# Optimization experiments

Hardware: AMD Instinct MI355X
Metric: run time of the kernel (lower is better)

The kernel has to match this reference:

```python
import jax, jax.numpy as jnp
import numpy as np

EPS = 1e-5

def setup_inputs() -> dict:
    key = jax.random.key(0)
    B, T, C, H = 1, 4096, 1024, 16
    ks = jax.random.split(key, 8)
    s = lambda k, sh, fan: jax.random.normal(k, sh, jnp.float32) * (1.0 / np.sqrt(fan))
    return {
        'x': jax.random.normal(ks[0], (B, T, C), jnp.float32),
        'ln1_g': jnp.ones((C,), jnp.float32), 'ln1_b': jnp.zeros((C,), jnp.float32),
        'w_qkv': s(ks[1], (C, 3 * C), C), 'b_qkv': jnp.zeros((3 * C,), jnp.float32),
        'w_out': s(ks[2], (C, C), C), 'b_out': jnp.zeros((C,), jnp.float32),
        'ln2_g': jnp.ones((C,), jnp.float32), 'ln2_b': jnp.zeros((C,), jnp.float32),
        'w_fc1': s(ks[3], (C, 4 * C), C), 'b_fc1': jnp.zeros((4 * C,), jnp.float32),
        'w_fc2': s(ks[4], (4 * C, C), 4 * C), 'b_fc2': jnp.zeros((C,), jnp.float32),
    }

def _layernorm(x, g, b):
    mu = jnp.mean(x, axis=-1, keepdims=True)
    var = jnp.mean(jnp.square(x - mu), axis=-1, keepdims=True)
    return (x - mu) * jax.lax.rsqrt(var + EPS) * g + b

def reference(x, ln1_g, ln1_b, w_qkv, b_qkv, w_out, b_out, ln2_g, ln2_b, w_fc1, b_fc1, w_fc2, b_fc2):
    B, T, C = x.shape
    H = 16
    D = C // H
    xn = _layernorm(x, ln1_g, ln1_b)
    qkv = xn @ w_qkv + b_qkv                      # [B,T,3C]
    qkv = qkv.reshape(B, T, 3, H, D).transpose(2, 0, 3, 1, 4)  # [3,B,H,T,D]
    q, k, v = qkv[0], qkv[1], qkv[2]
    scores = jnp.einsum('bhtd,bhsd->bhts', q, k) / jnp.sqrt(jnp.float32(D))
    mask = jnp.tril(jnp.ones((T, T), bool))
    scores = jnp.where(mask[None, None], scores, -jnp.inf)
    w = jax.nn.softmax(scores, axis=-1)
    attn = jnp.einsum('bhts,bhsd->bhtd', w, v)    # [B,H,T,D]
    attn = attn.transpose(0, 2, 1, 3).reshape(B, T, C)
    x = x + attn @ w_out + b_out
    xn2 = _layernorm(x, ln2_g, ln2_b)
    h = jax.nn.gelu(xn2 @ w_fc1 + b_fc1, approximate=False)
    return x + h @ w_fc2 + b_fc2
```

## Files before the change

kernel.cpp:

```cpp
#include <hip/hip_runtime.h>
#include <hip/hip_bf16.h>
#include <math.h>

typedef __attribute__((ext_vector_type(8))) short bf16x8;
typedef __attribute__((ext_vector_type(4))) float f32x4;
typedef unsigned short ushort_t;

#define T_SEQ 4096
#define C_DIM 1024
#define NH 16
#define HD 64

__device__ __forceinline__ ushort_t f2b(float f) {
  union { float f; unsigned u; } v; v.f = f;
  unsigned r = v.u + 0x7FFF + ((v.u >> 16) & 1);
  return (ushort_t)(r >> 16);
}

__global__ __launch_bounds__(256) void cast_transpose(const float* __restrict__ W,
                                                      ushort_t* __restrict__ WT,
                                                      int K, int N) {
  __shared__ ushort_t tile[32][40];
  int n0 = blockIdx.x * 32, k0 = blockIdx.y * 32;
  int t = threadIdx.x;
  int kl = t >> 3, nl = (t & 7) * 4;
  float4 v = *(const float4*)(W + (size_t)(k0 + kl) * N + n0 + nl);
  ushort4 c;
  c.x = f2b(v.x); c.y = f2b(v.y); c.z = f2b(v.z); c.w = f2b(v.w);
  *(ushort4*)&tile[kl][nl] = c;
  __syncthreads();
  int nl2 = t >> 3, kl2 = (t & 7) * 4;
  ushort4 o;
  o.x = tile[kl2 + 0][nl2];
  o.y = tile[kl2 + 1][nl2];
  o.z = tile[kl2 + 2][nl2];
  o.w = tile[kl2 + 3][nl2];
  *(ushort4*)(WT + (size_t)(n0 + nl2) * K + k0 + kl2) = o;
}

__global__ __launch_bounds__(256) void ln_kernel(const float* __restrict__ x,
                                                 const float* __restrict__ g,
                                                 const float* __restrict__ b,
                                                 ushort_t* __restrict__ out) {
  int row = blockIdx.x;
  int tid = threadIdx.x;
  float4 v = ((const float4*)(x + (size_t)row * C_DIM))[tid];
  float s  = v.x + v.y + v.z + v.w;
  float sq = v.x*v.x + v.y*v.y + v.z*v.z + v.w*v.w;
  #pragma unroll
  for (int m = 32; m >= 1; m >>= 1) {
    s  += __shfl_down(s, m, 64);
    sq += __shfl_down(sq, m, 64);
  }
  __shared__ float red[8];
  int wid = tid >> 6, lane = tid & 63;
  if (lane == 0) { red[wid] = s; red[wid + 4] = sq; }
  __syncthreads();
  s  = red[0] + red[1] + red[2] + red[3];
  sq = red[4] + red[5] + red[6] + red[7];
  float mu   = s * (1.0f / C_DIM);
  float var  = sq * (1.0f / C_DIM) - mu * mu;
  float rstd = rsqrtf(var + 1e-5f);
  float4 gg = ((const float4*)g)[tid];
  float4 bb = ((const float4*)b)[tid];
  ushort4 o;
  o.x = f2b((v.x - mu) * rstd * gg.x + bb.x);
  o.y = f2b((v.y - mu) * rstd * gg.y + bb.y);
  o.z = f2b((v.z - mu) * rstd * gg.z + bb.z);
  o.w = f2b((v.w - mu) * rstd * gg.w + bb.w);
  ((ushort4*)(out + (size_t)row * C_DIM))[tid] = o;
}

template<bool GELU, bool OUT_F32, bool RES>
__global__ __launch_bounds__(256) void gemm_bt(
    const ushort_t* __restrict__ A, const ushort_t* __restrict__ BT,
    const float* __restrict__ bias, const float* __restrict__ res,
    float* __restrict__ outF, ushort_t* __restrict__ outB,
    int M, int N, int K) {
  __shared__ ushort_t As[128][64];
  __shared__ ushort_t Bs[128][64];
  int tid  = threadIdx.x;
  int lane = tid & 63, w = tid >> 6;
  int wr = (w >> 1) * 64, wc = (w & 1) * 64;
  int brow = blockIdx.y * 128, bcol = blockIdx.x * 128;
  int l15 = lane & 15, lg = lane >> 4;

  f32x4 acc[4][4];
  #pragma unroll
  for (int m = 0; m < 4; ++m)
    #pragma unroll
    for (int n = 0; n < 4; ++n)
      acc[m][n] = (f32x4){0.f, 0.f, 0.f, 0.f};

  for (int k0 = 0; k0 < K; k0 += 64) {
    #pragma unroll
    for (int it = 0; it < 4; ++it) {
      int idx = it * 256 + tid;
      int r = idx >> 3, c = (idx & 7) * 8;
      __builtin_amdgcn_global_load_lds(
          (const __attribute__((address_space(1))) unsigned*)(A + (size_t)(brow + r) * K + k0 + c),
          (__attribute__((address_space(3))) unsigned*)&As[0][0] + idx * 4,
          16, 0, 0);
    }
    #pragma unroll
    for (int it = 0; it < 4; ++it) {
      int idx = it * 256 + tid;
      int r = idx >> 3, c = (idx & 7) * 8;
      __builtin_amdgcn_global_load_lds(
          (const __attribute__((address_space(1))) unsigned*)(BT + (size_t)(bcol + r) * K + k0 + c),
          (__attribute__((address_space(3))) unsigned*)&Bs[0][0] + idx * 4,
          16, 0, 0);
    }
    __syncthreads();
    #pragma unroll
    for (int half = 0; half < 2; ++half) {
      bf16x8 af[4], bfr[4];
      #pragma unroll
      for (int m = 0; m < 4; ++m)
        af[m] = *(const bf16x8*)&As[wr + m * 16 + l15][half * 32 + lg * 8];
      #pragma unroll
      for (int n = 0; n < 4; ++n)
        bfr[n] = *(const bf16x8*)&Bs[wc + n * 16 + l15][half * 32 + lg * 8];
      #pragma unroll
      for (int m = 0; m < 4; ++m)
        #pragma unroll
        for (int n = 0; n < 4; ++n)
          acc[m][n] = __builtin_amdgcn_mfma_f32_16x16x32_bf16(af[m], bfr[n], acc[m][n], 0, 0, 0);
    }
    __syncthreads();
  }

  #pragma unroll
  for (int m = 0; m < 4; ++m) {
    int row0 = brow + wr + m * 16 + lg * 4;
    #pragma unroll
    for (int n = 0; n < 4; ++n) {
      int col = bcol + wc + n * 16 + l15;
      float bv = bias[col];
      #pragma unroll
      for (int r = 0; r < 4; ++r) {
        int row = row0 + r;
        float v = acc[m][n][r] + bv;
        if (RES)  v += res[(size_t)row * N + col];
        if (GELU) v = 0.5f * v * (1.0f + erff(v * 0.70710678118f));
        if (OUT_F32) outF[(size_t)row * N + col] = v;
        else         outB[(size_t)row * N + col] = f2b(v);
      }
    }
  }
}

__global__ __launch_bounds__(256) void attn_kernel(const ushort_t* __restrict__ qkv,
                                                   float* __restrict__ part_O,
                                                   float* __restrict__ part_ml) {
  __shared__ ushort_t Ks[128][64];
  __shared__ ushort_t Vs[64][128];
  __shared__ ushort_t Pb[4][16][136];
  int h = blockIdx.y;
  int c = blockIdx.x;
  int qb, split, nsplit;
  if (c < 16)      { qb = c;                split = 0;           nsplit = 1; }
  else if (c < 48) { qb = 16 + ((c - 16) >> 1); split = (c - 16) & 1; nsplit = 2; }
  else if (c < 96) { qb = 32 + (c - 48) / 3;    split = (c - 48) % 3; nsplit = 3; }
  else             { qb = 48 + ((c - 96) >> 2); split = (c - 96) & 3; nsplit = 4; }
  int niter = (qb >> 1) + 1;
  int qd = niter / nsplit, rem = niter % nsplit;
  int it0 = split * qd + (split < rem ? split : rem);
  int itn = qd + (split < rem ? 1 : 0);

  int tid = threadIdx.x, lane = tid & 63, w = tid >> 6;
  int l15 = lane & 15, lg = lane >> 4;

  bf16x8 qf[2];
  {
    int qrow = qb * 64 + w * 16 + l15;
    const ushort_t* qp = qkv + (size_t)qrow * 3072 + h * 64;
    qf[0] = *(const bf16x8*)(qp + lg * 8);
    qf[1] = *(const bf16x8*)(qp + 32 + lg * 8);
  }
  float m_r[4], l_r[4];
  f32x4 o[4];
  #pragma unroll
  for (int r = 0; r < 4; ++r) { m_r[r] = -1e30f; l_r[r] = 0.f; }
  #pragma unroll
  for (int f = 0; f < 4; ++f) o[f] = (f32x4){0.f, 0.f, 0.f, 0.f};

  for (int s = it0; s < it0 + itn; ++s) {
    const ushort_t* kbase = qkv + (size_t)(s * 128) * 3072 + h * 64 + 1024;
    const ushort_t* vbase = kbase + 1024;
    #pragma unroll
    for (int it = 0; it < 4; ++it) {
      int idx = it * 256 + tid;
      int r = idx >> 3, ch = idx & 7;
      int srcc = (ch ^ (r & 7)) * 8;
      __builtin_amdgcn_global_load_lds(
          (const __attribute__((address_space(1))) unsigned*)(kbase + (size_t)r * 3072 + srcc),
          (__attribute__((address_space(3))) unsigned*)&Ks[0][0] + idx * 4,
          16, 0, 0);
    }
    #pragma unroll
    for (int it = 0; it < 4; ++it) {
      int idx = it * 256 + tid;
      int kv = (idx & 63) | ((idx >> 9) << 6);
      int d0 = ((idx >> 6) & 7) * 8;
      bf16x8 vv = *(const bf16x8*)(vbase + (size_t)kv * 3072 + d0);
      #pragma unroll
      for (int e = 0; e < 8; ++e)
        Vs[d0 + e][kv ^ (e << 3)] = ((ushort_t*)&vv)[e];
    }
    __syncthreads();

    f32x4 sf[8];
    #pragma unroll
    for (int f = 0; f < 8; ++f) {
      int row = f * 16 + l15;
      bf16x8 k0 = *(const bf16x8*)&Ks[row][(lg ^ (row & 7)) * 8];
      bf16x8 k1 = *(const bf16x8*)&Ks[row][((4 + lg) ^ (row & 7)) * 8];
      f32x4 a = (f32x4){0.f, 0.f, 0.f, 0.f};
      a = __builtin_amdgcn_mfma_f32_16x16x32_bf16(qf[0], k0, a, 0, 0, 0);
      a = __builtin_amdgcn_mfma_f32_16x16x32_bf16(qf[1], k1, a, 0, 0, 0);
      sf[f] = a;
    }

    float p[8][4];
    #pragma unroll
    for (int f = 0; f < 8; ++f)
      #pragma unroll
      for (int r = 0; r < 4; ++r) {
        float v = sf[f][r] * 0.125f;
        if (s == niter - 1) {
          int rl = qb * 64 + w * 16 + lg * 4 + r;
          int cl = s * 128 + f * 16 + l15;
          if (cl > rl) v = -1e30f;
        }
        p[f][r] = v;
      }

    #pragma unroll
    for (int r = 0; r < 4; ++r) {
      float mx = p[0][r];
      #pragma unroll
      for (int f = 1; f < 8; ++f) mx = fmaxf(mx, p[f][r]);
      #pragma unroll
      for (int off = 1; off < 16; off <<= 1) mx = fmaxf(mx, __shfl_xor(mx, off, 64));
      float mn = fmaxf(m_r[r], mx);
      float sc = __expf(m_r[r] - mn);
      float sum = 0.f;
      #pragma unroll
      for (int f = 0; f < 8; ++f) { p[f][r] = __expf(p[f][r] - mn); sum += p[f][r]; }
      #pragma unroll
      for (int off = 1; off < 16; off <<= 1) sum += __shfl_xor(sum, off, 64);
      l_r[r] = l_r[r] * sc + sum;
      m_r[r] = mn;
      #pragma unroll
      for (int f = 0; f < 4; ++f) o[f][r] *= sc;
    }

    #pragma unroll
    for (int f = 0; f < 8; ++f)
      #pragma unroll
      for (int r = 0; r < 4; ++r)
        Pb[w][lg * 4 + r][f * 16 + l15] = f2b(p[f][r]);

    #pragma unroll
    for (int kc = 0; kc < 4; ++kc) {
      bf16x8 pf = *(const bf16x8*)&Pb[w][l15][kc * 32 + lg * 8];
      #pragma unroll
      for (int f = 0; f < 4; ++f) {
        int d = f * 16 + l15;
        bf16x8 vf = *(const bf16x8*)&Vs[d][(((kc * 4) + lg) ^ (d & 7)) * 8];
        o[f] = __builtin_amdgcn_mfma_f32_16x16x32_bf16(pf, vf, o[f], 0, 0, 0);
      }
    }
    __syncthreads();
  }

  int pidx = h * 160 + c;
  float* po = part_O + (size_t)pidx * 4096;
  #pragma unroll
  for (int f = 0; f < 4; ++f)
    #pragma unroll
    for (int r = 0; r < 4; ++r)
      po[(w * 16 + lg * 4 + r) * 64 + f * 16 + l15] = o[f][r];
  if (l15 == 0) {
    float* pm = part_ml + (size_t)pidx * 128;
    #pragma unroll
    for (int r = 0; r < 4; ++r) {
      int row = w * 16 + lg * 4 + r;
      pm[row]      = m_r[r];
      pm[64 + row] = l_r[r];
    }
  }
}

__global__ __launch_bounds__(256) void attn_merge(const float* __restrict__ part_O,
                                                  const float* __restrict__ part_ml,
                                                  ushort_t* __restrict__ out) {
  int qb = blockIdx.x, h = blockIdx.y;
  int nsplit, base;
  if (qb < 16)      { nsplit = 1; base = qb; }
  else if (qb < 32) { nsplit = 2; base = 16 + 2 * (qb - 16); }
  else if (qb < 48) { nsplit = 3; base = 48 + 3 * (qb - 32); }
  else              { nsplit = 4; base = 96 + 4 * (qb - 48); }
  int t = threadIdx.x;
  int r = t >> 2, d0 = (t & 3) * 16;
  int p0 = h * 160 + base;

  float mv0 = part_ml[(size_t)p0 * 128 + r];
  float lv0 = part_ml[(size_t)p0 * 128 + 64 + r];
  float mv1 = nsplit > 1 ? part_ml[(size_t)(p0 + 1) * 128 + r]      : -1e30f;
  float lv1 = nsplit > 1 ? part_ml[(size_t)(p0 + 1) * 128 + 64 + r] : 0.f;
  float mv2 = nsplit > 2 ? part_ml[(size_t)(p0 + 2) * 128 + r]      : -1e30f;
  float lv2 = nsplit > 2 ? part_ml[(size_t)(p0 + 2) * 128 + 64 + r] : 0.f;
  float mv3 = nsplit > 3 ? part_ml[(size_t)(p0 + 3) * 128 + r]      : -1e30f;
  float lv3 = nsplit > 3 ? part_ml[(size_t)(p0 + 3) * 128 + 64 + r] : 0.f;
  float M = fmaxf(fmaxf(mv0, mv1), fmaxf(mv2, mv3));
  float s0 = __expf(mv0 - M), s1 = __expf(mv1 - M);
  float s2 = __expf(mv2 - M), s3 = __expf(mv3 - M);
  float L = lv0 * s0 + lv1 * s1 + lv2 * s2 + lv3 * s3;
  float inv = 1.0f / L;

  float acc[16];
  #pragma unroll
  for (int e = 0; e < 16; ++e) acc[e] = 0.f;
  {
    const float* po = part_O + (size_t)p0 * 4096 + r * 64 + d0;
    #pragma unroll
    for (int e = 0; e < 16; e += 4) {
      float4 v = *(const float4*)(po + e);
      acc[e] += v.x * s0; acc[e+1] += v.y * s0; acc[e+2] += v.z * s0; acc[e+3] += v.w * s0;
    }
  }
  if (nsplit > 1) {
    const float* po = part_O + (size_t)(p0 + 1) * 4096 + r * 64 + d0;
    #pragma unroll
    for (int e = 0; e < 16; e += 4) {
      float4 v = *(const float4*)(po + e);
      acc[e] += v.x * s1; acc[e+1] += v.y * s1; acc[e+2] += v.z * s1; acc[e+3] += v.w * s1;
    }
  }
  if (nsplit > 2) {
    const float* po = part_O + (size_t)(p0 + 2) * 4096 + r * 64 + d0;
    #pragma unroll
    for (int e = 0; e < 16; e += 4) {
      float4 v = *(const float4*)(po + e);
      acc[e] += v.x * s2; acc[e+1] += v.y * s2; acc[e+2] += v.z * s2; acc[e+3] += v.w * s2;
    }
  }
  if (nsplit > 3) {
    const float* po = part_O + (size_t)(p0 + 3) * 4096 + r * 64 + d0;
    #pragma unroll
    for (int e = 0; e < 16; e += 4) {
      float4 v = *(const float4*)(po + e);
      acc[e] += v.x * s3; acc[e+1] += v.y * s3; acc[e+2] += v.z * s3; acc[e+3] += v.w * s3;
    }
  }

  ushort_t* op = out + (size_t)(qb * 64 + r) * C_DIM + h * 64 + d0;
  #pragma unroll
  for (int e = 0; e < 16; ++e) op[e] = f2b(acc[e] * inv);
}

extern "C" void kernel_launch(void* const* d_in, const int* in_sizes, int n_in,
                              void* d_out, int out_size, void* d_ws, size_t ws_size,
                              hipStream_t stream) {
  const float* x     = (const float*)d_in[0];
  const float* ln1_g = (const float*)d_in[1];
  const float* ln1_b = (const float*)d_in[2];
  const float* w_qkv = (const float*)d_in[3];
  const float* b_qkv = (const float*)d_in[4];
  const float* w_out = (const float*)d_in[5];
  const float* b_out = (const float*)d_in[6];
  const float* ln2_g = (const float*)d_in[7];
  const float* ln2_b = (const float*)d_in[8];
  const float* w_fc1 = (const float*)d_in[9];
  const float* b_fc1 = (const float*)d_in[10];
  const float* w_fc2 = (const float*)d_in[11];
  const float* b_fc2 = (const float*)d_in[12];

  char* ws = (char*)d_ws;
  size_t off = 0;
  auto alloc = [&](size_t bytes) {
    void* p = ws + off;
    off = (off + bytes + 255) & ~(size_t)255;
    return p;
  };
  ushort_t* wqkvT = (ushort_t*)alloc((size_t)3 * C_DIM * C_DIM * 2);
  ushort_t* woutT = (ushort_t*)alloc((size_t)C_DIM * C_DIM * 2);
  ushort_t* wfc1T = (ushort_t*)alloc((size_t)4 * C_DIM * C_DIM * 2);
  ushort_t* wfc2T = (ushort_t*)alloc((size_t)C_DIM * 4 * C_DIM * 2);
  ushort_t* xn1   = (ushort_t*)alloc((size_t)T_SEQ * C_DIM * 2);
  ushort_t* qkv   = (ushort_t*)alloc((size_t)T_SEQ * 3 * C_DIM * 2);
  ushort_t* attnO = (ushort_t*)alloc((size_t)T_SEQ * C_DIM * 2);
  float*    x2    = (float*)   alloc((size_t)T_SEQ * C_DIM * 4);
  ushort_t* xn2   = (ushort_t*)alloc((size_t)T_SEQ * C_DIM * 2);
  ushort_t* hbuf  = (ushort_t*)alloc((size_t)T_SEQ * 4 * C_DIM * 2);
  (void)ws_size;
  float* part_O  = (float*)x2;
  float* part_ml = (float*)((char*)x2 + (size_t)2560 * 4096 * 4);

  cast_transpose<<<dim3(96, 32),  256, 0, stream>>>(w_qkv, wqkvT, C_DIM, 3 * C_DIM);
  cast_transpose<<<dim3(32, 32),  256, 0, stream>>>(w_out, woutT, C_DIM, C_DIM);
  cast_transpose<<<dim3(128, 32), 256, 0, stream>>>(w_fc1, wfc1T, C_DIM, 4 * C_DIM);
  cast_transpose<<<dim3(32, 128), 256, 0, stream>>>(w_fc2, wfc2T, 4 * C_DIM, C_DIM);

  ln_kernel<<<dim3(T_SEQ), 256, 0, stream>>>(x, ln1_g, ln1_b, xn1);

  gemm_bt<false, false, false><<<dim3(24, 32), 256, 0, stream>>>(
      xn1, wqkvT, b_qkv, nullptr, nullptr, qkv, T_SEQ, 3 * C_DIM, C_DIM);

  attn_kernel<<<dim3(160, NH), 256, 0, stream>>>(qkv, part_O, part_ml);
  attn_merge<<<dim3(T_SEQ / 64, NH), 256, 0, stream>>>(part_O, part_ml, attnO);

  gemm_bt<false, true, true><<<dim3(8, 32), 256, 0, stream>>>(
      attnO, woutT, b_out, x, x2, nullptr, T_SEQ, C_DIM, C_DIM);

  ln_kernel<<<dim3(T_SEQ), 256, 0, stream>>>(x2, ln2_g, ln2_b, xn2);

  gemm_bt<true, false, false><<<dim3(32, 32), 256, 0, stream>>>(
      xn2, wfc1T, b_fc1, nullptr, nullptr, hbuf, T_SEQ, 4 * C_DIM, C_DIM);

  gemm_bt<false, true, true><<<dim3(8, 32), 256, 0, stream>>>(
      hbuf, wfc2T, b_fc2, x2, (float*)d_out, nullptr, T_SEQ, C_DIM, 4 * C_DIM);
}
```

Measured before the change: 547.5 us.

## Double-buffer GEMM LDS tiles and transpose attention scores for cheaper softmax

Result: faster. 478.2 us (-12.7%).

```diff
diff --git a/kernel.cpp b/kernel.cpp
--- a/kernel.cpp
+++ b/kernel.cpp
@@ -77,8 +77,8 @@
     const float* __restrict__ bias, const float* __restrict__ res,
     float* __restrict__ outF, ushort_t* __restrict__ outB,
     int M, int N, int K) {
-  __shared__ ushort_t As[128][64];
-  __shared__ ushort_t Bs[128][64];
+  __shared__ ushort_t As[2][128][32];
+  __shared__ ushort_t Bs[2][128][32];
   int tid  = threadIdx.x;
   int lane = tid & 63, w = tid >> 6;
   int wr = (w >> 1) * 64, wc = (w & 1) * 64;
@@ -92,41 +92,45 @@
     for (int n = 0; n < 4; ++n)
       acc[m][n] = (f32x4){0.f, 0.f, 0.f, 0.f};
 
-  for (int k0 = 0; k0 < K; k0 += 64) {
-    #pragma unroll
-    for (int it = 0; it < 4; ++it) {
+  auto stage = [&](int buf, int k0) {
+    #pragma unroll
+    for (int it = 0; it < 2; ++it) {
       int idx = it * 256 + tid;
-      int r = idx >> 3, c = (idx & 7) * 8;
+      int r = idx >> 2, c = (idx & 3) * 8;
       __builtin_amdgcn_global_load_lds(
           (const __attribute__((address_space(1))) unsigned*)(A + (size_t)(brow + r) * K + k0 + c),
-          (__attribute__((address_space(3))) unsigned*)&As[0][0] + idx * 4,
+          (__attribute__((address_space(3))) unsigned*)&As[buf][0][0] + idx * 4,
           16, 0, 0);
     }
     #pragma unroll
-    for (int it = 0; it < 4; ++it) {
+    for (int it = 0; it < 2; ++it) {
       int idx = it * 256 + tid;
-      int r = idx >> 3, c = (idx & 7) * 8;
+      int r = idx >> 2, c = (idx & 3) * 8;
       __builtin_amdgcn_global_load_lds(
           (const __attribute__((address_space(1))) unsigned*)(BT + (size_t)(bcol + r) * K + k0 + c),
-          (__attribute__((address_space(3))) unsigned*)&Bs[0][0] + idx * 4,
+          (__attribute__((address_space(3))) unsigned*)&Bs[buf][0][0] + idx * 4,
           16, 0, 0);
     }
-    __syncthreads();
-    #pragma unroll
-    for (int half = 0; half < 2; ++half) {
-      bf16x8 af[4], bfr[4];
-      #pragma unroll
-      for (int m = 0; m < 4; ++m)
-        af[m] = *(const bf16x8*)&As[wr + m * 16 + l15][half * 32 + lg * 8];
+  };
+
+  int nt = K >> 5;
+  stage(0, 0);
+  __syncthreads();
+  for (int t = 0; t < nt; ++t) {
+    if (t + 1 < nt) stage((t + 1) & 1, (t + 1) << 5);
+    int cur = t & 1;
+    bf16x8 af[4], bfr[4];
+    #pragma unroll
+    for (int m = 0; m < 4; ++m)
+      af[m] = *(const bf16x8*)&As[cur][wr + m * 16 + l15][lg * 8];
+    #pragma unroll
+    for (int n = 0; n < 4; ++n)
+      bfr[n] = *(const bf16x8*)&Bs[cur][wc + n * 16 + l15][lg * 8];
+    #pragma unroll
+    for (int m = 0; m < 4; ++m)
       #pragma unroll
       for (int n = 0; n < 4; ++n)
-        bfr[n] = *(const bf16x8*)&Bs[wc + n * 16 + l15][half * 32 + lg * 8];
-      #pragma unroll
-      for (int m = 0; m < 4; ++m)
-        #pragma unroll
-        for (int n = 0; n < 4; ++n)
-          acc[m][n] = __builtin_amdgcn_mfma_f32_16x16x32_bf16(af[m], bfr[n], acc[m][n], 0, 0, 0);
-    }
+        acc[m][n] = __builtin_amdgcn_mfma_f32_16x16x32_bf16(af[m], bfr[n], acc[m][n], 0, 0, 0);
     __syncthreads();
   }
 
@@ -178,10 +182,8 @@
     qf[0] = *(const bf16x8*)(qp + lg * 8);
     qf[1] = *(const bf16x8*)(qp + 32 + lg * 8);
   }
-  float m_r[4], l_r[4];
+  float m_l = -1e30f, l_l = 0.f;
   f32x4 o[4];
-  #pragma unroll
-  for (int r = 0; r < 4; ++r) { m_r[r] = -1e30f; l_r[r] = 0.f; }
   #pragma unroll
   for (int f = 0; f < 4; ++f) o[f] = (f32x4){0.f, 0.f, 0.f, 0.f};
 
@@ -210,57 +212,62 @@
     }
     __syncthreads();
 
-    f32x4 sf[8];
+    float p[8][4];
     #pragma unroll
     for (int f = 0; f < 8; ++f) {
-      int row = f * 16 + l15;
-      bf16x8 k0 = *(const bf16x8*)&Ks[row][(lg ^ (row & 7)) * 8];
-      bf16x8 k1 = *(const bf16x8*)&Ks[row][((4 + lg) ^ (row & 7)) * 8];
+      int kvrow = f * 16 + l15;
+      bf16x8 k0 = *(const bf16x8*)&Ks[kvrow][(lg ^ (kvrow & 7)) * 8];
+      bf16x8 k1 = *(const bf16x8*)&Ks[kvrow][((4 + lg) ^ (kvrow & 7)) * 8];
       f32x4 a = (f32x4){0.f, 0.f, 0.f, 0.f};
-      a = __builtin_amdgcn_mfma_f32_16x16x32_bf16(qf[0], k0, a, 0, 0, 0);
-      a = __builtin_amdgcn_mfma_f32_16x16x32_bf16(qf[1], k1, a, 0, 0, 0);
-      sf[f] = a;
-    }
-
-    float p[8][4];
-    #pragma unroll
-    for (int f = 0; f < 8; ++f)
+      a = __builtin_amdgcn_mfma_f32_16x16x32_bf16(k0, qf[0], a, 0, 0, 0);
+      a = __builtin_amdgcn_mfma_f32_16x16x32_bf16(k1, qf[1], a, 0, 0, 0);
       #pragma unroll
       for (int r = 0; r < 4; ++r) {
-        float v = sf[f][r] * 0.125f;
+        float v = a[r] * 0.125f;
         if (s == niter - 1) {
-          int rl = qb * 64 + w * 16 + lg * 4 + r;
-          int cl = s * 128 + f * 16 + l15;
+          int cl = s * 128 + f * 16 + lg * 4 + r;
+          int rl = qb * 64 + w * 16 + l15;
           if (cl > rl) v = -1e30f;
         }
         p[f][r] = v;
       }
+    }
+
+    float mx = p[0][0];
+    #pragma unroll
+    for (int f = 0; f < 8; ++f)
+      #pragma unroll
+      for (int r = 0; r < 4; ++r) mx = fmaxf(mx, p[f][r]);
+    mx = fmaxf(mx, __shfl_xor(mx, 16, 64));
+    mx = fmaxf(mx, __shfl_xor(mx, 32, 64));
+    float mn = fmaxf(m_l, mx);
+    float sc = __expf(m_l - mn);
+    m_l = mn;
+    float sum = 0.f;
+    #pragma unroll
+    for (int f = 0; f < 8; ++f)
+      #pragma unroll
+      for (int r = 0; r < 4; ++r) { p[f][r] = __expf(p[f][r] - mn); sum += p[f][r]; }
+    sum += __shfl_xor(sum, 16, 64);
+    sum += __shfl_xor(sum, 32, 64);
+    l_l = l_l * sc + sum;
 
     #pragma unroll
     for (int r = 0; r < 4; ++r) {
-      float mx = p[0][r];
-      #pragma unroll
-      for (int f = 1; f < 8; ++f) mx = fmaxf(mx, p[f][r]);
-      #pragma unroll
-      for (int off = 1; off < 16; off <<= 1) mx = fmaxf(mx, __shfl_xor(mx, off, 64));
-      float mn = fmaxf(m_r[r], mx);
-      float sc = __expf(m_r[r] - mn);
-      float sum = 0.f;
-      #pragma unroll
-      for (int f = 0; f < 8; ++f) { p[f][r] = __expf(p[f][r] - mn); sum += p[f][r]; }
-      #pragma unroll
-      for (int off = 1; off < 16; off <<= 1) sum += __shfl_xor(sum, off, 64);
-      l_r[r] = l_r[r] * sc + sum;
-      m_r[r] = mn;
-      #pragma unroll
-      for (int f = 0; f < 4; ++f) o[f][r] *= sc;
-    }
-
-    #pragma unroll
-    for (int f = 0; f < 8; ++f)
-      #pragma unroll
-      for (int r = 0; r < 4; ++r)
-        Pb[w][lg * 4 + r][f * 16 + l15] = f2b(p[f][r]);
+      float scr = __shfl(sc, lg * 4 + r, 64);
+      #pragma unroll
+      for (int f = 0; f < 4; ++f) o[f][r] *= scr;
+    }
+
+    #pragma unroll
+    for (int f = 0; f < 8; ++f) {
+      #pragma unroll
+      for (int rp = 0; rp < 2; ++rp) {
+        unsigned u;
+        asm("v_cvt_pk_bf16_f32 %0, %1, %2" : "=v"(u) : "v"(p[f][2 * rp]), "v"(p[f][2 * rp + 1]));
+        *(unsigned*)&Pb[w][l15][f * 16 + lg * 4 + 2 * rp] = u;
+      }
+    }
 
     #pragma unroll
     for (int kc = 0; kc < 4; ++kc) {
@@ -282,14 +289,10 @@
     #pragma unroll
     for (int r = 0; r < 4; ++r)
       po[(w * 16 + lg * 4 + r) * 64 + f * 16 + l15] = o[f][r];
-  if (l15 == 0) {
+  if (lane < 16) {
     float* pm = part_ml + (size_t)pidx * 128;
-    #pragma unroll
-    for (int r = 0; r < 4; ++r) {
-      int row = w * 16 + lg * 4 + r;
-      pm[row]      = m_r[r];
-      pm[64 + row] = l_r[r];
-    }
+    pm[w * 16 + lane]      = m_l;
+    pm[64 + w * 16 + lane] = l_l;
   }
 }
 
```
